# Kernel optimization log

Measured on AMD Instinct MI355X. Metric: run time of the kernel, lower is better.

## Reference

```python
import jax, jax.numpy as jnp
import numpy as np

B, T, C, H = 2, 2048, 1024, 16
HS = C // H  # head size = 64


def _rope_cos_sin(t, hs):
    # theta_i = 1/10000^(2(i-1)/hs) for i in [1, hs/2]
    pos = jnp.arange(t, dtype=jnp.float32)[:, None]          # [T,1]
    i = jnp.arange(1, hs // 2 + 1, dtype=jnp.float32)[None]  # [1,hs/2]
    theta = 1.0 / 10000.0 ** (2.0 * (i - 1.0) / hs)
    ang = pos * theta                                        # [T,hs/2]
    return jnp.cos(ang), jnp.sin(ang)


def _apply_rope(u, cos, sin):
    # u: [B,H,T,HS]; complex multiply on consecutive pairs
    u2 = u.reshape(*u.shape[:-1], HS // 2, 2)
    x0, x1 = u2[..., 0], u2[..., 1]
    c = cos[None, None]  # [1,1,T,hs/2]
    s = sin[None, None]
    r0 = x0 * c - x1 * s
    r1 = x0 * s + x1 * c
    return jnp.stack([r0, r1], axis=-1).reshape(u.shape)


def setup_inputs() -> dict:
    key = jax.random.key(0)
    ks = jax.random.split(key, 5)
    return {
        "x": jax.random.normal(ks[0], (B, T, C), dtype=jnp.float32),
        "W_qkv": jax.random.normal(ks[1], (C, 3 * C), dtype=jnp.float32) * 0.02,
        "b_qkv": jax.random.normal(ks[2], (3 * C,), dtype=jnp.float32) * 0.02,
        "W_proj": jax.random.normal(ks[3], (C, C), dtype=jnp.float32) * 0.02,
        "b_proj": jax.random.normal(ks[4], (C,), dtype=jnp.float32) * 0.02,
    }


def reference(x, W_qkv, b_qkv, W_proj, b_proj):
    b, t, c = x.shape
    qkv = x @ W_qkv + b_qkv                                   # [B,T,3C]
    qkv = qkv.reshape(b, t, H, 3 * HS).transpose(0, 2, 1, 3)  # [B,H,T,3*HS]
    q, k, v = jnp.split(qkv, 3, axis=-1)                      # each [B,H,T,HS]

    cos, sin = _rope_cos_sin(t, HS)
    q = _apply_rope(q, cos, sin)
    k = _apply_rope(k, cos, sin)

    att = jnp.einsum("bhqd,bhkd->bhqk", q, k) / jnp.sqrt(jnp.float32(HS))
    causal = jnp.tril(jnp.ones((t, t), dtype=bool))[None, None]
    att = jnp.where(causal, att, jnp.float32(-1e9))
    att = jax.nn.softmax(att, axis=-1)
    y = jnp.einsum("bhqk,bhkd->bhqd", att, v)                 # [B,H,T,HS]
    y = y.transpose(0, 2, 1, 3).reshape(b, t, c)
    return y @ W_proj + b_proj
```

## Files before the change

kernel.cpp:

```cpp
#include <hip/hip_runtime.h>

typedef unsigned short u16;
typedef unsigned int u32;
typedef __bf16 bf16x8 __attribute__((ext_vector_type(8)));
typedef float f32x4 __attribute__((ext_vector_type(4)));
typedef u16 u16x4 __attribute__((ext_vector_type(4)));
typedef u16 u16x8 __attribute__((ext_vector_type(8)));

__device__ __forceinline__ u16 f2bf(float f) {
  u32 u = __builtin_bit_cast(u32, f);
  u += 0x7fffu + ((u >> 16) & 1u);
  return (u16)(u >> 16);
}

__device__ __forceinline__ void gld16(const void* g, void* l) {
  __builtin_amdgcn_global_load_lds(
      (const __attribute__((address_space(1))) void*)g,
      (__attribute__((address_space(3))) void*)l, 16, 0, 0);
}

__global__ __launch_bounds__(256) void k_conv_x(const float* __restrict__ x,
                                                u16* __restrict__ xb) {
  int i = (blockIdx.x * 256 + threadIdx.x) * 4;
  float4 v = *(const float4*)(x + i);
  u16x4 o = { f2bf(v.x), f2bf(v.y), f2bf(v.z), f2bf(v.w) };
  *(u16x4*)(xb + i) = o;
}

__global__ __launch_bounds__(256) void k_transpose(const float* __restrict__ src,
                                                   u16* __restrict__ dst,
                                                   int R, int Cc) {
  __shared__ float tile[32][33];
  int x = threadIdx.x & 31, y = threadIdx.x >> 5;
  int c0 = blockIdx.x * 32, r0 = blockIdx.y * 32;
  for (int i = 0; i < 4; ++i)
    tile[y + 8 * i][x] = src[(size_t)(r0 + y + 8 * i) * Cc + c0 + x];
  __syncthreads();
  for (int i = 0; i < 4; ++i)
    dst[(size_t)(c0 + y + 8 * i) * R + r0 + x] = f2bf(tile[x][y + 8 * i]);
}

__global__ __launch_bounds__(256) void k_rope_tab(float2* __restrict__ tab) {
  int i = blockIdx.x * 256 + threadIdx.x;
  int t = i >> 5, d = i & 31;
  float theta = expf(-(float)d * 0.28782313662425575f);
  float ang = (float)t * theta;
  tab[i] = make_float2(cosf(ang), sinf(ang));
}

__global__ __launch_bounds__(256) void k_qkv(
    const u16* __restrict__ Xb,
    const u16* __restrict__ Wt,
    const float* __restrict__ bias,
    const float2* __restrict__ rope,
    u16* __restrict__ Qg,
    u16* __restrict__ Kg,
    u16* __restrict__ Vt) {
  __shared__ alignas(16) u16 As[128 * 32];
  __shared__ alignas(16) u16 Bs[128 * 32];
  __shared__ alignas(16) u16 Es[2][9216];
  const int tid = threadIdx.x;
  const int lane = tid & 63, w = tid >> 6;
  const int quad = lane >> 4, l15 = lane & 15;
  const int m0 = blockIdx.y * 128, n0 = blockIdx.x * 128;
  const int lr = lane >> 2, lc = (lane & 3) * 8;
  const int wm = (w & 1) * 64, wn = (w >> 1) * 64;
  const f32x4 vzero = {0.f, 0.f, 0.f, 0.f};

  f32x4 acc[4][4];
  for (int i = 0; i < 4; ++i)
    for (int j = 0; j < 4; ++j) acc[i][j] = vzero;

  for (int kt = 0; kt < 1024; kt += 32) {
    __syncthreads();
    for (int i = 0; i < 2; ++i) {
      int row = w * 32 + i * 16;
      gld16(Xb + (size_t)(m0 + row + lr) * 1024 + kt + lc, &As[row * 32]);
      gld16(Wt + (size_t)(n0 + row + lr) * 1024 + kt + lc, &Bs[row * 32]);
    }
    __syncthreads();
    bf16x8 a[4], b[4];
    for (int mt = 0; mt < 4; ++mt)
      a[mt] = *(const bf16x8*)&As[(wm + mt * 16 + l15) * 32 + quad * 8];
    for (int nt = 0; nt < 4; ++nt)
      b[nt] = *(const bf16x8*)&Bs[(wn + nt * 16 + l15) * 32 + quad * 8];
    for (int mt = 0; mt < 4; ++mt)
      for (int nt = 0; nt < 4; ++nt)
        acc[mt][nt] = __builtin_amdgcn_mfma_f32_16x16x32_bf16(
            a[mt], b[nt], acc[mt][nt], 0, 0, 0);
  }

  {
    const int half = w >> 1;
    const int nh = n0 + half * 64;
    const int pbase = nh % 192;
    const int region = pbase >> 6;
    for (int nt = 0; nt < 4; ++nt) {
      int c = nt * 16 + l15;
      float bv = bias[nh + c];
      for (int mt = 0; mt < 4; ++mt) {
        for (int r = 0; r < 4; ++r) {
          int m_l = wm + mt * 16 + quad * 4 + r;
          float v = acc[mt][nt][r] + bv;
          float partner = __shfl_xor(v, 1, 64);
          if (region < 2) {
            int t = (m0 + m_l) & 2047;
            float2 cs = rope[t * 32 + (c >> 1)];
            float outv = (c & 1) ? fmaf(partner, cs.y, v * cs.x)
                                 : fmaf(-partner, cs.y, v * cs.x);
            Es[half][m_l * 72 + c] = f2bf(outv);
          } else {
            Es[half][c * 136 + m_l] = f2bf(v);
          }
        }
      }
    }
  }
  __syncthreads();

  const int bb = m0 >> 11, t0 = m0 & 2047;
  for (int hf = 0; hf < 2; ++hf) {
    const int nh = n0 + hf * 64;
    const int hh = nh / 192;
    const int region = (nh % 192) >> 6;
    if (region < 2) {
      u16* dst = (region == 0 ? Qg : Kg) +
                 ((size_t)(bb * 16 + hh) * 2048 + t0) * 64;
      int chunk = tid & 7, row0 = tid >> 3;
      for (int p = 0; p < 4; ++p) {
        int row = row0 + p * 32;
        u16x8 val = *(const u16x8*)&Es[hf][row * 72 + chunk * 8];
        *(u16x8*)(dst + (size_t)row * 64 + chunk * 8) = val;
      }
    } else {
      u16* dstv = Vt + (size_t)(bb * 16 + hh) * 64 * 2048 + t0;
      int mch = tid & 15, c0r = tid >> 4;
      for (int p = 0; p < 4; ++p) {
        int c = c0r + p * 16;
        u16x8 val = *(const u16x8*)&Es[hf][c * 136 + mch * 8];
        *(u16x8*)(dstv + (size_t)c * 2048 + mch * 8) = val;
      }
    }
  }
}

__global__ __launch_bounds__(512, 4) void k_attn(
    const u16* __restrict__ Qg, const u16* __restrict__ Kg,
    const u16* __restrict__ Vt, u16* __restrict__ Og) {
  __shared__ alignas(16) u16 Ks[64 * 64];
  __shared__ alignas(16) u16 Vs[64 * 64];
  __shared__ alignas(16) u16 Ps[128 * 72];
  const int tid = threadIdx.x, lane = tid & 63, w = tid >> 6;
  const int quad = lane >> 4, l15 = lane & 15;
  const int bh = blockIdx.y;
  int tmp = (blockIdx.x + bh) & 15;
  const int qt = (bh & 16) ? (15 - tmp) : tmp;
  const int q0 = qt * 128;
  const u16* Qh = Qg + (size_t)bh * 2048 * 64;
  const u16* Kh = Kg + (size_t)bh * 2048 * 64;
  const u16* Vh = Vt + (size_t)bh * 64 * 2048;
  const f32x4 vzero = {0.f, 0.f, 0.f, 0.f};
  const float SCL = 0.125f * 1.4426950408889634f;

  bf16x8 aq[2];
  {
    const u16* qp = Qh + (size_t)(q0 + w * 16 + l15) * 64 + quad * 8;
    aq[0] = *(const bf16x8*)(qp);
    aq[1] = *(const bf16x8*)(qp + 32);
  }

  const int r8 = lane >> 3, j8 = lane & 7;
  const int sw_c = (j8 ^ r8) * 8;

  float lsum[4] = {0.f, 0.f, 0.f, 0.f};
  f32x4 O[4];
  for (int nt = 0; nt < 4; ++nt) O[nt] = vzero;

  const int nk = 2 * qt + 2;
  for (int kb = 0; kb < nk; ++kb) {
    int k0 = kb * 64;
    __syncthreads();
    gld16(Kh + (size_t)(k0 + w * 8 + r8) * 64 + sw_c, &Ks[w * 8 * 64]);
    gld16(Vh + (size_t)(w * 8 + r8) * 2048 + k0 + sw_c, &Vs[w * 8 * 64]);
    __syncthreads();

    if (k0 <= q0 + w * 16 + 15) {
      f32x4 s[4];
      for (int nt = 0; nt < 4; ++nt) s[nt] = vzero;
      for (int ks = 0; ks < 2; ++ks) {
        bf16x8 b[4];
        for (int nt = 0; nt < 4; ++nt)
          b[nt] = *(const bf16x8*)&Ks[(nt * 16 + l15) * 64 +
                                      ((ks * 4 + quad) ^ (l15 & 7)) * 8];
        for (int nt = 0; nt < 4; ++nt)
          s[nt] = __builtin_amdgcn_mfma_f32_16x16x32_bf16(aq[ks], b[nt], s[nt], 0, 0, 0);
      }

      const bool anymask = (k0 + 63 > q0 + w * 16);
      for (int r = 0; r < 4; ++r) {
        int prow = w * 16 + quad * 4 + r;
        int tq = q0 + prow;
        float acc_l = 0.f;
        for (int nt = 0; nt < 4; ++nt) {
          float pv = __builtin_amdgcn_exp2f(s[nt][r] * SCL);
          if (anymask && (k0 + nt * 16 + l15 > tq)) pv = 0.f;
          acc_l += pv;
          Ps[prow * 72 + nt * 16 + l15] = f2bf(pv);
        }
        lsum[r] += acc_l;
      }

      for (int ks = 0; ks < 2; ++ks) {
        bf16x8 a = *(const bf16x8*)&Ps[(w * 16 + l15) * 72 + ks * 32 + quad * 8];
        bf16x8 b[4];
        for (int nt = 0; nt < 4; ++nt)
          b[nt] = *(const bf16x8*)&Vs[(nt * 16 + l15) * 64 +
                                      ((ks * 4 + quad) ^ (l15 & 7)) * 8];
        for (int nt = 0; nt < 4; ++nt)
          O[nt] = __builtin_amdgcn_mfma_f32_16x16x32_bf16(a, b[nt], O[nt], 0, 0, 0);
      }
    }
  }

  float inv[4];
  for (int r = 0; r < 4; ++r) {
    float v = lsum[r];
    for (int msk = 1; msk < 16; msk <<= 1) v += __shfl_xor(v, msk, 64);
    inv[r] = 1.0f / v;
  }

  __syncthreads();
  for (int nt = 0; nt < 4; ++nt)
    for (int r = 0; r < 4; ++r)
      Ps[(w * 16 + quad * 4 + r) * 72 + nt * 16 + l15] = f2bf(O[nt][r] * inv[r]);
  __syncthreads();
  const int bb = bh >> 4, h = bh & 15;
  u16* dst = Og + ((size_t)bb * 2048 + q0) * 1024 + h * 64;
  int chunk = tid & 7, row0 = tid >> 3;
  for (int p = 0; p < 2; ++p) {
    int row = row0 + p * 64;
    u16x8 val = *(const u16x8*)&Ps[row * 72 + chunk * 8];
    *(u16x8*)(dst + (size_t)row * 1024 + chunk * 8) = val;
  }
}

__global__ __launch_bounds__(256) void k_proj(
    const u16* __restrict__ Ag,
    const u16* __restrict__ Wt,
    const float* __restrict__ bias,
    float* __restrict__ out) {
  __shared__ alignas(16) u16 As[128 * 32];
  __shared__ alignas(16) u16 Bs[128 * 32];
  const int tid = threadIdx.x;
  const int lane = tid & 63, w = tid >> 6;
  const int quad = lane >> 4, l15 = lane & 15;
  const int m0 = blockIdx.y * 128, n0 = blockIdx.x * 128;
  const int lr = lane >> 2, lc = (lane & 3) * 8;
  const int wm = (w & 1) * 64, wn = (w >> 1) * 64;
  const f32x4 vzero = {0.f, 0.f, 0.f, 0.f};

  f32x4 acc[4][4];
  for (int i = 0; i < 4; ++i)
    for (int j = 0; j < 4; ++j) acc[i][j] = vzero;

  for (int kt = 0; kt < 1024; kt += 32) {
    __syncthreads();
    for (int i = 0; i < 2; ++i) {
      int row = w * 32 + i * 16;
      gld16(Ag + (size_t)(m0 + row + lr) * 1024 + kt + lc, &As[row * 32]);
      gld16(Wt + (size_t)(n0 + row + lr) * 1024 + kt + lc, &Bs[row * 32]);
    }
    __syncthreads();
    bf16x8 a[4], b[4];
    for (int mt = 0; mt < 4; ++mt)
      a[mt] = *(const bf16x8*)&As[(wm + mt * 16 + l15) * 32 + quad * 8];
    for (int nt = 0; nt < 4; ++nt)
      b[nt] = *(const bf16x8*)&Bs[(wn + nt * 16 + l15) * 32 + quad * 8];
    for (int mt = 0; mt < 4; ++mt)
      for (int nt = 0; nt < 4; ++nt)
        acc[mt][nt] = __builtin_amdgcn_mfma_f32_16x16x32_bf16(
            a[mt], b[nt], acc[mt][nt], 0, 0, 0);
  }

  for (int nt = 0; nt < 4; ++nt) {
    int n = n0 + wn + nt * 16 + l15;
    float bv = bias[n];
    for (int mt = 0; mt < 4; ++mt)
      for (int r = 0; r < 4; ++r) {
        int m = m0 + wm + mt * 16 + quad * 4 + r;
        out[(size_t)m * 1024 + n] = acc[mt][nt][r] + bv;
      }
  }
}

extern "C" void kernel_launch(void* const* d_in, const int* in_sizes, int n_in,
                              void* d_out, int out_size, void* d_ws, size_t ws_size,
                              hipStream_t stream) {
  (void)in_sizes; (void)n_in; (void)out_size; (void)ws_size;
  const float* x     = (const float*)d_in[0];
  const float* Wqkv  = (const float*)d_in[1];
  const float* bqkv  = (const float*)d_in[2];
  const float* Wproj = (const float*)d_in[3];
  const float* bproj = (const float*)d_in[4];
  float* out = (float*)d_out;

  char* ws = (char*)d_ws;
  size_t off = 0;
  u16* Xb    = (u16*)(ws + off); off += (size_t)4096 * 1024 * 2;
  u16* Wqkvt = (u16*)(ws + off); off += (size_t)3072 * 1024 * 2;
  u16* Wpt   = (u16*)(ws + off); off += (size_t)1024 * 1024 * 2;
  u16* Qg    = (u16*)(ws + off); off += (size_t)2 * 16 * 2048 * 64 * 2;
  u16* Kg    = (u16*)(ws + off); off += (size_t)2 * 16 * 2048 * 64 * 2;
  u16* Vt    = (u16*)(ws + off); off += (size_t)2 * 16 * 64 * 2048 * 2;
  u16* Att   = (u16*)(ws + off); off += (size_t)4096 * 1024 * 2;
  float2* rope = (float2*)(ws + off); off += (size_t)2048 * 32 * sizeof(float2);

  k_conv_x<<<4096, 256, 0, stream>>>(x, Xb);
  k_transpose<<<dim3(96, 32), 256, 0, stream>>>(Wqkv, Wqkvt, 1024, 3072);
  k_transpose<<<dim3(32, 32), 256, 0, stream>>>(Wproj, Wpt, 1024, 1024);
  k_rope_tab<<<256, 256, 0, stream>>>(rope);
  k_qkv<<<dim3(24, 32), 256, 0, stream>>>(Xb, Wqkvt, bqkv, rope, Qg, Kg, Vt);
  k_attn<<<dim3(16, 32), 512, 0, stream>>>(Qg, Kg, Vt, Att);
  k_proj<<<dim3(8, 32), 256, 0, stream>>>(Att, Wpt, bproj, out);
}
```

Measured before the change: 206.8 us.

## Fuse prep kernels, double-buffer K/V in attention, transpose score MFMA

Merges the four preprocessing launches (x conversion, two weight transposes, rope table) into one kernel to cut launch overhead. In attention, K/V tiles are double-buffered so the next tile loads while the current one is computed, dropping one barrier per iteration. The score MFMA operands are swapped so each lane holds a query row, which allows packed bf16 stores of P and a cheaper row-sum reduction. V epilogue stores in qkv are also packed. The pk2 rounding is simpler than round-to-nearest-even, and the early continue still reaches the barrier at the top of the loop.

Measured after the change: 196.6 us. 1.05x faster.

```diff
diff --git a/kernel.cpp b/kernel.cpp
--- a/kernel.cpp
+++ b/kernel.cpp
@@ -13,39 +13,55 @@
   return (u16)(u >> 16);
 }
 
+__device__ __forceinline__ u32 pk2(float a, float b) {
+  u32 ua = __builtin_bit_cast(u32, a) + 0x8000u;
+  u32 ub = __builtin_bit_cast(u32, b) + 0x8000u;
+  return __builtin_amdgcn_perm(ub, ua, 0x07060302);
+}
+
 __device__ __forceinline__ void gld16(const void* g, void* l) {
   __builtin_amdgcn_global_load_lds(
       (const __attribute__((address_space(1))) void*)g,
       (__attribute__((address_space(3))) void*)l, 16, 0, 0);
 }
 
-__global__ __launch_bounds__(256) void k_conv_x(const float* __restrict__ x,
-                                                u16* __restrict__ xb) {
-  int i = (blockIdx.x * 256 + threadIdx.x) * 4;
-  float4 v = *(const float4*)(x + i);
-  u16x4 o = { f2bf(v.x), f2bf(v.y), f2bf(v.z), f2bf(v.w) };
-  *(u16x4*)(xb + i) = o;
-}
-
-__global__ __launch_bounds__(256) void k_transpose(const float* __restrict__ src,
-                                                   u16* __restrict__ dst,
-                                                   int R, int Cc) {
+__global__ __launch_bounds__(256) void k_prep(
+    const float* __restrict__ x, u16* __restrict__ xb,
+    const float* __restrict__ Wqkv, u16* __restrict__ Wqkvt,
+    const float* __restrict__ Wproj, u16* __restrict__ Wpt,
+    float2* __restrict__ rope) {
   __shared__ float tile[32][33];
-  int x = threadIdx.x & 31, y = threadIdx.x >> 5;
-  int c0 = blockIdx.x * 32, r0 = blockIdx.y * 32;
+  const int tid = threadIdx.x;
+  int bx = blockIdx.x;
+  if (bx < 4096) {
+    int i = (bx * 256 + tid) * 4;
+    float4 v = *(const float4*)(x + i);
+    u16x4 o = { f2bf(v.x), f2bf(v.y), f2bf(v.z), f2bf(v.w) };
+    *(u16x4*)(xb + i) = o;
+    return;
+  }
+  bx -= 4096;
+  const float* src; u16* dst; int R, Cc, bxx, byy;
+  if (bx < 3072) {
+    src = Wqkv; dst = Wqkvt; R = 1024; Cc = 3072; bxx = bx % 96; byy = bx / 96;
+  } else if (bx < 4096) {
+    int b = bx - 3072;
+    src = Wproj; dst = Wpt; R = 1024; Cc = 1024; bxx = b % 32; byy = b / 32;
+  } else {
+    int i = (bx - 4096) * 256 + tid;
+    int t = i >> 5, d = i & 31;
+    float theta = expf(-(float)d * 0.28782313662425575f);
+    float ang = (float)t * theta;
+    rope[i] = make_float2(cosf(ang), sinf(ang));
+    return;
+  }
+  int xx = tid & 31, yy = tid >> 5;
+  int c0 = bxx * 32, r0 = byy * 32;
   for (int i = 0; i < 4; ++i)
-    tile[y + 8 * i][x] = src[(size_t)(r0 + y + 8 * i) * Cc + c0 + x];
+    tile[yy + 8 * i][xx] = src[(size_t)(r0 + yy + 8 * i) * Cc + c0 + xx];
   __syncthreads();
   for (int i = 0; i < 4; ++i)
-    dst[(size_t)(c0 + y + 8 * i) * R + r0 + x] = f2bf(tile[x][y + 8 * i]);
-}
-
-__global__ __launch_bounds__(256) void k_rope_tab(float2* __restrict__ tab) {
-  int i = blockIdx.x * 256 + threadIdx.x;
-  int t = i >> 5, d = i & 31;
-  float theta = expf(-(float)d * 0.28782313662425575f);
-  float ang = (float)t * theta;
-  tab[i] = make_float2(cosf(ang), sinf(ang));
+    dst[(size_t)(c0 + yy + 8 * i) * R + r0 + xx] = f2bf(tile[xx][yy + 8 * i]);
 }
 
 __global__ __launch_bounds__(256) void k_qkv(
@@ -93,25 +109,33 @@
   {
     const int half = w >> 1;
     const int nh = n0 + half * 64;
-    const int pbase = nh % 192;
-    const int region = pbase >> 6;
-    for (int nt = 0; nt < 4; ++nt) {
-      int c = nt * 16 + l15;
-      float bv = bias[nh + c];
-      for (int mt = 0; mt < 4; ++mt) {
-        for (int r = 0; r < 4; ++r) {
-          int m_l = wm + mt * 16 + quad * 4 + r;
-          float v = acc[mt][nt][r] + bv;
-          float partner = __shfl_xor(v, 1, 64);
-          if (region < 2) {
+    const int region = (nh % 192) >> 6;
+    if (region < 2) {
+      for (int nt = 0; nt < 4; ++nt) {
+        int c = nt * 16 + l15;
+        float bv = bias[nh + c];
+        for (int mt = 0; mt < 4; ++mt) {
+          for (int r = 0; r < 4; ++r) {
+            int m_l = wm + mt * 16 + quad * 4 + r;
+            float v = acc[mt][nt][r] + bv;
+            float partner = __shfl_xor(v, 1, 64);
             int t = (m0 + m_l) & 2047;
             float2 cs = rope[t * 32 + (c >> 1)];
             float outv = (c & 1) ? fmaf(partner, cs.y, v * cs.x)
                                  : fmaf(-partner, cs.y, v * cs.x);
             Es[half][m_l * 72 + c] = f2bf(outv);
-          } else {
-            Es[half][c * 136 + m_l] = f2bf(v);
           }
+        }
+      }
+    } else {
+      for (int nt = 0; nt < 4; ++nt) {
+        int c = nt * 16 + l15;
+        float bv = bias[nh + c];
+        for (int mt = 0; mt < 4; ++mt) {
+          float v0 = acc[mt][nt][0] + bv, v1 = acc[mt][nt][1] + bv;
+          float v2 = acc[mt][nt][2] + bv, v3 = acc[mt][nt][3] + bv;
+          uint2 pv; pv.x = pk2(v0, v1); pv.y = pk2(v2, v3);
+          *(uint2*)&Es[half][c * 136 + wm + mt * 16 + quad * 4] = pv;
         }
       }
     }
@@ -147,8 +171,8 @@
 __global__ __launch_bounds__(512, 4) void k_attn(
     const u16* __restrict__ Qg, const u16* __restrict__ Kg,
     const u16* __restrict__ Vt, u16* __restrict__ Og) {
-  __shared__ alignas(16) u16 Ks[64 * 64];
-  __shared__ alignas(16) u16 Vs[64 * 64];
+  __shared__ alignas(16) u16 Ks[2][64 * 64];
+  __shared__ alignas(16) u16 Vs[2][64 * 64];
   __shared__ alignas(16) u16 Ps[128 * 72];
   const int tid = threadIdx.x, lane = tid & 63, w = tid >> 6;
   const int quad = lane >> 4, l15 = lane & 15;
@@ -161,10 +185,11 @@
   const u16* Vh = Vt + (size_t)bh * 64 * 2048;
   const f32x4 vzero = {0.f, 0.f, 0.f, 0.f};
   const float SCL = 0.125f * 1.4426950408889634f;
+  const int myrow = w * 16;
 
   bf16x8 aq[2];
   {
-    const u16* qp = Qh + (size_t)(q0 + w * 16 + l15) * 64 + quad * 8;
+    const u16* qp = Qh + (size_t)(q0 + myrow + l15) * 64 + quad * 8;
     aq[0] = *(const bf16x8*)(qp);
     aq[1] = *(const bf16x8*)(qp + 32);
   }
@@ -172,67 +197,81 @@
   const int r8 = lane >> 3, j8 = lane & 7;
   const int sw_c = (j8 ^ r8) * 8;
 
-  float lsum[4] = {0.f, 0.f, 0.f, 0.f};
+  float lsum = 0.f;
   f32x4 O[4];
   for (int nt = 0; nt < 4; ++nt) O[nt] = vzero;
 
   const int nk = 2 * qt + 2;
+  gld16(Kh + (size_t)(w * 8 + r8) * 64 + sw_c, &Ks[0][w * 8 * 64]);
+  gld16(Vh + (size_t)(w * 8 + r8) * 2048 + sw_c, &Vs[0][w * 8 * 64]);
+
   for (int kb = 0; kb < nk; ++kb) {
-    int k0 = kb * 64;
-    __syncthreads();
-    gld16(Kh + (size_t)(k0 + w * 8 + r8) * 64 + sw_c, &Ks[w * 8 * 64]);
-    gld16(Vh + (size_t)(w * 8 + r8) * 2048 + k0 + sw_c, &Vs[w * 8 * 64]);
-    __syncthreads();
-
-    if (k0 <= q0 + w * 16 + 15) {
-      f32x4 s[4];
-      for (int nt = 0; nt < 4; ++nt) s[nt] = vzero;
-      for (int ks = 0; ks < 2; ++ks) {
-        bf16x8 b[4];
-        for (int nt = 0; nt < 4; ++nt)
-          b[nt] = *(const bf16x8*)&Ks[(nt * 16 + l15) * 64 +
-                                      ((ks * 4 + quad) ^ (l15 & 7)) * 8];
-        for (int nt = 0; nt < 4; ++nt)
-          s[nt] = __builtin_amdgcn_mfma_f32_16x16x32_bf16(aq[ks], b[nt], s[nt], 0, 0, 0);
-      }
-
-      const bool anymask = (k0 + 63 > q0 + w * 16);
-      for (int r = 0; r < 4; ++r) {
-        int prow = w * 16 + quad * 4 + r;
-        int tq = q0 + prow;
-        float acc_l = 0.f;
-        for (int nt = 0; nt < 4; ++nt) {
-          float pv = __builtin_amdgcn_exp2f(s[nt][r] * SCL);
-          if (anymask && (k0 + nt * 16 + l15 > tq)) pv = 0.f;
-          acc_l += pv;
-          Ps[prow * 72 + nt * 16 + l15] = f2bf(pv);
+    const int k0 = kb * 64;
+    const int cur = kb & 1;
+    __syncthreads();
+    if (kb + 1 < nk) {
+      const int k1 = k0 + 64;
+      gld16(Kh + (size_t)(k1 + w * 8 + r8) * 64 + sw_c, &Ks[cur ^ 1][w * 8 * 64]);
+      gld16(Vh + (size_t)(w * 8 + r8) * 2048 + k1 + sw_c, &Vs[cur ^ 1][w * 8 * 64]);
+    }
+    if (k0 > q0 + myrow + 15) continue;
+
+    f32x4 st[4];
+    for (int nt = 0; nt < 4; ++nt) st[nt] = vzero;
+    for (int ks = 0; ks < 2; ++ks) {
+      bf16x8 ak[4];
+      for (int nt = 0; nt < 4; ++nt)
+        ak[nt] = *(const bf16x8*)&Ks[cur][(nt * 16 + l15) * 64 +
+                                         ((ks * 4 + quad) ^ (l15 & 7)) * 8];
+      for (int nt = 0; nt < 4; ++nt)
+        st[nt] = __builtin_amdgcn_mfma_f32_16x16x32_bf16(ak[nt], aq[ks], st[nt], 0, 0, 0);
+    }
+
+    if (k0 + 63 <= q0 + myrow) {
+      for (int nt = 0; nt < 4; ++nt) {
+        float p0 = __builtin_amdgcn_exp2f(st[nt][0] * SCL);
+        float p1 = __builtin_amdgcn_exp2f(st[nt][1] * SCL);
+        float p2 = __builtin_amdgcn_exp2f(st[nt][2] * SCL);
+        float p3 = __builtin_amdgcn_exp2f(st[nt][3] * SCL);
+        lsum += (p0 + p1) + (p2 + p3);
+        uint2 pv; pv.x = pk2(p0, p1); pv.y = pk2(p2, p3);
+        *(uint2*)&Ps[(myrow + l15) * 72 + nt * 16 + quad * 4] = pv;
+      }
+    } else {
+      const int tq = q0 + myrow + l15;
+      const int kbase = k0 + quad * 4;
+      for (int nt = 0; nt < 4; ++nt) {
+        float p[4];
+        for (int r = 0; r < 4; ++r) {
+          float pv = __builtin_amdgcn_exp2f(st[nt][r] * SCL);
+          p[r] = (kbase + nt * 16 + r <= tq) ? pv : 0.f;
+          lsum += p[r];
         }
-        lsum[r] += acc_l;
-      }
-
-      for (int ks = 0; ks < 2; ++ks) {
-        bf16x8 a = *(const bf16x8*)&Ps[(w * 16 + l15) * 72 + ks * 32 + quad * 8];
-        bf16x8 b[4];
-        for (int nt = 0; nt < 4; ++nt)
-          b[nt] = *(const bf16x8*)&Vs[(nt * 16 + l15) * 64 +
-                                      ((ks * 4 + quad) ^ (l15 & 7)) * 8];
-        for (int nt = 0; nt < 4; ++nt)
-          O[nt] = __builtin_amdgcn_mfma_f32_16x16x32_bf16(a, b[nt], O[nt], 0, 0, 0);
-      }
-    }
-  }
-
+        uint2 pv; pv.x = pk2(p[0], p[1]); pv.y = pk2(p[2], p[3]);
+        *(uint2*)&Ps[(myrow + l15) * 72 + nt * 16 + quad * 4] = pv;
+      }
+    }
+
+    for (int ks = 0; ks < 2; ++ks) {
+      bf16x8 a = *(const bf16x8*)&Ps[(myrow + l15) * 72 + ks * 32 + quad * 8];
+      bf16x8 bv[4];
+      for (int nt = 0; nt < 4; ++nt)
+        bv[nt] = *(const bf16x8*)&Vs[cur][(nt * 16 + l15) * 64 +
+                                         ((ks * 4 + quad) ^ (l15 & 7)) * 8];
+      for (int nt = 0; nt < 4; ++nt)
+        O[nt] = __builtin_amdgcn_mfma_f32_16x16x32_bf16(a, bv[nt], O[nt], 0, 0, 0);
+    }
+  }
+
+  lsum += __shfl_xor(lsum, 16, 64);
+  lsum += __shfl_xor(lsum, 32, 64);
   float inv[4];
-  for (int r = 0; r < 4; ++r) {
-    float v = lsum[r];
-    for (int msk = 1; msk < 16; msk <<= 1) v += __shfl_xor(v, msk, 64);
-    inv[r] = 1.0f / v;
-  }
-
-  __syncthreads();
+  for (int r = 0; r < 4; ++r)
+    inv[r] = 1.0f / __shfl(lsum, quad * 4 + r, 16);
+
   for (int nt = 0; nt < 4; ++nt)
     for (int r = 0; r < 4; ++r)
-      Ps[(w * 16 + quad * 4 + r) * 72 + nt * 16 + l15] = f2bf(O[nt][r] * inv[r]);
+      Ps[(myrow + quad * 4 + r) * 72 + nt * 16 + l15] = f2bf(O[nt][r] * inv[r]);
   __syncthreads();
   const int bb = bh >> 4, h = bh & 15;
   u16* dst = Og + ((size_t)bb * 2048 + q0) * 1024 + h * 64;
@@ -315,10 +354,7 @@
   u16* Att   = (u16*)(ws + off); off += (size_t)4096 * 1024 * 2;
   float2* rope = (float2*)(ws + off); off += (size_t)2048 * 32 * sizeof(float2);
 
-  k_conv_x<<<4096, 256, 0, stream>>>(x, Xb);
-  k_transpose<<<dim3(96, 32), 256, 0, stream>>>(Wqkv, Wqkvt, 1024, 3072);
-  k_transpose<<<dim3(32, 32), 256, 0, stream>>>(Wproj, Wpt, 1024, 1024);
-  k_rope_tab<<<256, 256, 0, stream>>>(rope);
+  k_prep<<<8448, 256, 0, stream>>>(x, Xb, Wqkv, Wqkvt, Wproj, Wpt, rope);
   k_qkv<<<dim3(24, 32), 256, 0, stream>>>(Xb, Wqkvt, bqkv, rope, Qg, Kg, Vt);
   k_attn<<<dim3(16, 32), 512, 0, stream>>>(Qg, Kg, Vt, Att);
   k_proj<<<dim3(8, 32), 256, 0, stream>>>(Att, Wpt, bproj, out);
```
